# Kernel tuning notes

Hardware: AMD Instinct MI355X
Metric: run time of the kernel (lower is better)

## Reference

```python
import jax, jax.numpy as jnp
import numpy as np

SQRT_2_OVER_PI = 0.79788456

def gelu_tanh(x):
    # tanh-approximate GELU, matches torch F.gelu(approximate='tanh')
    return 0.5 * x * (1.0 + jnp.tanh(SQRT_2_OVER_PI * x * (1.0 + 0.044715 * x * x)))

def gelu_bwd(x):
    # analytical derivative of tanh-approx GELU (same constants as source)
    t = jnp.tanh(SQRT_2_OVER_PI * x * (1.0 + 0.044715 * x * x))
    return 0.5 * x * ((1.0 - t * t) * (SQRT_2_OVER_PI + 0.1070322243 * x * x)) + 0.5 * (1.0 + t)

def setup_inputs() -> dict:
    key = jax.random.key(0)
    ks = jax.random.split(key, 6)
    T, d_phi, d_h = 8192, 4096, 64
    d_mid = 4 * d_h
    return {
        "phi_seq": jax.random.normal(ks[0], (T, d_phi), jnp.float32),
        "C_seq": jax.random.uniform(ks[1], (T,), jnp.float32),
        "theta_K_w": jax.random.normal(ks[2], (d_h, d_phi), jnp.float32) * 0.02,
        "theta_Q_w": jax.random.normal(ks[3], (d_h, d_phi), jnp.float32) * 0.02,
        "W10": jax.random.normal(ks[4], (d_h, d_mid), jnp.float32) * 0.02,
        "b10": jnp.zeros((d_mid,), jnp.float32),
        "W20": jax.random.normal(ks[5], (d_mid,), jnp.float32) * 0.02,
        "b20": jnp.zeros((), jnp.float32),
        "log_eta": jnp.asarray(np.log(0.01), jnp.float32),
    }

def reference(phi_seq, C_seq, theta_K_w, theta_Q_w, W10, b10, W20, b20, log_eta):
    eta = jnp.exp(log_eta)
    # Slow-weight projections hoisted out of the scan (same math, one big GEMM)
    u_Q = phi_seq @ theta_Q_w.T  # [T, d_h]
    u_K = phi_seq @ theta_K_w.T  # [T, d_h]

    def step(carry, inp):
        W1, b1, W2, b2 = carry
        u_q, u_k = inp
        # score with current fast weights
        s = jax.nn.sigmoid(gelu_tanh(u_q @ W1 + b1) @ W2 + b2)
        # update fast weights (inner objective, C_t = 0.0)
        Z1 = u_k @ W1 + b1          # [d_mid]
        X2 = gelu_tanh(Z1)
        pred = jax.nn.sigmoid(X2 @ W2 + b2)
        d_Z2 = 2.0 * pred * pred * (1.0 - pred)  # d/dZ2 of (pred-0)^2
        d_Z1 = (d_Z2 * W2) * gelu_bwd(Z1)
        new_carry = (
            W1 - eta * jnp.outer(u_k, d_Z1),
            b1 - eta * d_Z1,
            W2 - eta * d_Z2 * X2,
            b2 - eta * d_Z2,
        )
        return new_carry, s

    _, scores = jax.lax.scan(step, (W10, b10, W20, b20), (u_Q, u_K))
    outer_loss = jnp.sum((scores - C_seq) ** 2)
    return scores, outer_loss
```

## Files before the change

### kernel.cpp

```cpp
#include <hip/hip_runtime.h>
#include <hip/hip_bf16.h>

#define DH 64
#define DM 256

typedef float f32x2 __attribute__((ext_vector_type(2)));

__device__ __forceinline__ f32x2 sp2(float s) { return (f32x2){s, s}; }
__device__ __forceinline__ f32x2 pkfma(f32x2 a, f32x2 b, f32x2 c) {
#if __has_builtin(__builtin_elementwise_fma)
    return __builtin_elementwise_fma(a, b, c);
#else
    f32x2 r; r.x = fmaf(a.x, b.x, c.x); r.y = fmaf(a.y, b.y, c.y); return r;
#endif
}

__device__ __forceinline__ float tanh_fast(float y) {
    float e = __expf(2.0f * y);
    return 1.0f - 2.0f / (e + 1.0f);
}
__device__ __forceinline__ float sigmoid_fast(float x) {
    return 1.0f / (1.0f + __expf(-x));
}

template <int CTRL, int RMASK>
__device__ __forceinline__ float dpp_term(float x) {
    int p = __builtin_amdgcn_update_dpp(0, __float_as_int(x), CTRL, RMASK, 0xf, false);
    return __int_as_float(p);
}
__device__ __forceinline__ float wave_sum63(float x) {
    x += dpp_term<0xB1,  0xf>(x);
    x += dpp_term<0x4E,  0xf>(x);
    x += dpp_term<0x141, 0xf>(x);
    x += dpp_term<0x140, 0xf>(x);
    x += dpp_term<0x142, 0xa>(x);
    x += dpp_term<0x143, 0xc>(x);
    return x;
}

__global__ __launch_bounds__(256) void proj_kernel(
    const float* __restrict__ phi,
    const float* __restrict__ thK,
    const float* __restrict__ thQ,
    float* __restrict__ u,
    int dphi)
{
    const int tid  = threadIdx.x;
    const int th32 = tid & 31;
    const int tt8  = tid >> 5;
    const int t0   = tt8 * 4;
    const int h0   = th32 * 4;
    const int T0   = blockIdx.x * 32;

    __shared__ float sPhiT[32][36];
    __shared__ float sThT[32][128];

    const int h   = tid >> 1;
    const int ko  = (tid & 1) * 16;
    const float* trow = (h < 64) ? (thQ + (size_t)h * dphi)
                                 : (thK + (size_t)(h - 64) * dphi);
    const int tr  = tid >> 3;
    const int k4p = (tid & 7) * 4;

    float4 pv, tv0, tv1, tv2, tv3;
    pv  = *(const float4*)&phi[(size_t)(T0 + tr) * dphi + k4p];
    tv0 = *(const float4*)&trow[ko + 0];
    tv1 = *(const float4*)&trow[ko + 4];
    tv2 = *(const float4*)&trow[ko + 8];
    tv3 = *(const float4*)&trow[ko + 12];

    float acc[4][4];
    #pragma unroll
    for (int i = 0; i < 4; ++i)
        #pragma unroll
        for (int jj = 0; jj < 4; ++jj) acc[i][jj] = 0.0f;

    const int NC = dphi / 32;
    for (int c = 0; c < NC; ++c) {
        __syncthreads();
        sPhiT[k4p + 0][tr] = pv.x;
        sPhiT[k4p + 1][tr] = pv.y;
        sPhiT[k4p + 2][tr] = pv.z;
        sPhiT[k4p + 3][tr] = pv.w;
        sThT[ko +  0][h] = tv0.x;  sThT[ko +  1][h] = tv0.y;
        sThT[ko +  2][h] = tv0.z;  sThT[ko +  3][h] = tv0.w;
        sThT[ko +  4][h] = tv1.x;  sThT[ko +  5][h] = tv1.y;
        sThT[ko +  6][h] = tv1.z;  sThT[ko +  7][h] = tv1.w;
        sThT[ko +  8][h] = tv2.x;  sThT[ko +  9][h] = tv2.y;
        sThT[ko + 10][h] = tv2.z;  sThT[ko + 11][h] = tv2.w;
        sThT[ko + 12][h] = tv3.x;  sThT[ko + 13][h] = tv3.y;
        sThT[ko + 14][h] = tv3.z;  sThT[ko + 15][h] = tv3.w;
        __syncthreads();
        if (c + 1 < NC) {
            const int kb = (c + 1) * 32;
            pv  = *(const float4*)&phi[(size_t)(T0 + tr) * dphi + kb + k4p];
            tv0 = *(const float4*)&trow[kb + ko + 0];
            tv1 = *(const float4*)&trow[kb + ko + 4];
            tv2 = *(const float4*)&trow[kb + ko + 8];
            tv3 = *(const float4*)&trow[kb + ko + 12];
        }
        #pragma unroll 8
        for (int k = 0; k < 32; ++k) {
            float4 ph = *(const float4*)&sPhiT[k][t0];
            float4 th = *(const float4*)&sThT[k][h0];
            acc[0][0] = fmaf(ph.x, th.x, acc[0][0]);
            acc[0][1] = fmaf(ph.x, th.y, acc[0][1]);
            acc[0][2] = fmaf(ph.x, th.z, acc[0][2]);
            acc[0][3] = fmaf(ph.x, th.w, acc[0][3]);
            acc[1][0] = fmaf(ph.y, th.x, acc[1][0]);
            acc[1][1] = fmaf(ph.y, th.y, acc[1][1]);
            acc[1][2] = fmaf(ph.y, th.z, acc[1][2]);
            acc[1][3] = fmaf(ph.y, th.w, acc[1][3]);
            acc[2][0] = fmaf(ph.z, th.x, acc[2][0]);
            acc[2][1] = fmaf(ph.z, th.y, acc[2][1]);
            acc[2][2] = fmaf(ph.z, th.z, acc[2][2]);
            acc[2][3] = fmaf(ph.z, th.w, acc[2][3]);
            acc[3][0] = fmaf(ph.w, th.x, acc[3][0]);
            acc[3][1] = fmaf(ph.w, th.y, acc[3][1]);
            acc[3][2] = fmaf(ph.w, th.z, acc[3][2]);
            acc[3][3] = fmaf(ph.w, th.w, acc[3][3]);
        }
    }
    #pragma unroll
    for (int i = 0; i < 4; ++i) {
        float4 o;
        o.x = acc[i][0]; o.y = acc[i][1]; o.z = acc[i][2]; o.w = acc[i][3];
        *(float4*)&u[(size_t)(T0 + t0 + i) * 128 + h0] = o;
    }
}

__global__ __launch_bounds__(256) void dots_kernel(
    const float* __restrict__ u, float4* __restrict__ dd4, int T)
{
    const int t    = (blockIdx.x * 256 + threadIdx.x) >> 6;
    const int lane = threadIdx.x & 63;
    if (t >= T) return;
    float uq = u[(size_t)t * 128 + lane];
    float uk = u[(size_t)t * 128 + 64 + lane];
    float k1 = (t >= 1) ? u[(size_t)(t - 1) * 128 + 64 + lane] : 0.f;
    float k2 = (t >= 2) ? u[(size_t)(t - 2) * 128 + 64 + lane] : 0.f;
    float a = k1 * uq, b = k1 * uk, c = k2 * uq, d = k2 * uk;
    #pragma unroll
    for (int off = 32; off > 0; off >>= 1) {
        a += __shfl_xor(a, off);
        b += __shfl_xor(b, off);
        c += __shfl_xor(c, off);
        d += __shfl_xor(d, off);
    }
    if (lane == 0) dd4[t] = make_float4(a, b, c, d);
}


#define ROWU(uqs, uks, ums, i2) do {                                         \
    f32x2 wa_ = pkfma(sp2(-(ums)), e1g0_, w1p[i2]);                          \
    f32x2 wb_ = pkfma(sp2(-(ums)), e1g1_, w1p[(i2) + 1]);                    \
    w1p[i2] = wa_; w1p[(i2) + 1] = wb_;                                      \
    aq0_ = pkfma(sp2(uqs), wa_, aq0_);  aq1_ = pkfma(sp2(uqs), wb_, aq1_);   \
    ak0_ = pkfma(sp2(uks), wa_, ak0_);  ak1_ = pkfma(sp2(uks), wb_, ak1_);   \
} while (0)
#define ROWU4(q4, k4, m4, b) do {                                            \
    ROWU((q4).x, (k4).x, (m4).x, (b) + 0);                                   \
    ROWU((q4).y, (k4).y, (m4).y, (b) + 2);                                   \
    ROWU((q4).z, (k4).z, (m4).z, (b) + 4);                                   \
    ROWU((q4).w, (k4).w, (m4).w, (b) + 6);                                   \
} while (0)
#define ROWM(uqs, uks, i2) do {                                              \
    aq0_ = pkfma(sp2(uqs), w1p[i2], aq0_);                                   \
    aq1_ = pkfma(sp2(uqs), w1p[(i2) + 1], aq1_);                             \
    ak0_ = pkfma(sp2(uks), w1p[i2], ak0_);                                   \
    ak1_ = pkfma(sp2(uks), w1p[(i2) + 1], ak1_);                             \
} while (0)
#define ROWM4(q4, k4, b) do {                                                \
    ROWM((q4).x, (k4).x, (b) + 0);                                           \
    ROWM((q4).y, (k4).y, (b) + 2);                                           \
    ROWM((q4).z, (k4).z, (b) + 4);                                           \
    ROWM((q4).w, (k4).w, (b) + 6);                                           \
} while (0)

#define STEP(t_) do {                                                        \
    const int pbR_ = (t_) & 1;                                               \
    const int r_   = (t_) & 63;                                              \
    const int B_   = (t_) >> 6;                                              \
    const int bs_  = B_ & 1;                                                 \
                                               \
    float4 pqQ_ = *(const float4*)&pqk[pbR_ ^ 1][0];                         \
    float4 pqK_ = *(const float4*)&pqk[pbR_ ^ 1][4];                         \
    const int sE_ = ((t_) + 2) & 3;                                          \
    float eb0_ = ebufT[sE_][0][lane];                                        \
    float eb1_ = ebufT[sE_][1][lane];                                        \
    float eb2_ = ebufT[sE_][2][lane];                                        \
    float eb3_ = ebufT[sE_][3][lane];                                        \
    float4 ddv_ = *(const float4*)&dbuf[bs_][r_][0];                         \
    float pA0_ = pbuf[pbR_][0][0][j], pA1_ = pbuf[pbR_][1][0][j];            \
    float pA2_ = pbuf[pbR_][2][0][j], pA3_ = pbuf[pbR_][3][0][j];            \
    float pB0_ = pbuf[pbR_][0][1][j], pB1_ = pbuf[pbR_][1][1][j];            \
    float pB2_ = pbuf[pbR_][2][1][j], pB3_ = pbuf[pbR_][3][1][j];            \
    const int ci_ = ((t_) > 0) ? (t_) - 1 : 0;                               \
    float cv_ = cbuf[((ci_ >> 6) & 1) * 64 + (ci_ & 63)];                    \
    const int rn_ = ((t_) + 1 < T) ? (t_) + 1 : T - 1;                       \
    const float* urN_ = &ubuf[((rn_ >> 6) & 1) * 8192 + (rn_ & 63) * 128];   \
    float4 q40_ = *(const float4*)&urN_[uqo +  0];                           \
    float4 q41_ = *(const float4*)&urN_[uqo +  4];                           \
    float4 q42_ = *(const float4*)&urN_[uqo +  8];                           \
    float4 q43_ = *(const float4*)&urN_[uqo + 12];                           \
    float4 k40_ = *(const float4*)&urN_[uko +  0];                           \
    float4 k41_ = *(const float4*)&urN_[uko +  4];                           \
    float4 k42_ = *(const float4*)&urN_[uko +  8];                           \
    float4 k43_ = *(const float4*)&urN_[uko + 12];                           \
    const int tm2_ = ((t_) >= 2) ? (t_) - 2 : 0;                             \
    const float* urM_ = &ubuf[((tm2_ >> 6) & 1) * 8192 + (tm2_ & 63) * 128]; \
    float4 m40_ = *(const float4*)&urM_[uko +  0];                           \
    float4 m41_ = *(const float4*)&urM_[uko +  4];                           \
    float4 m42_ = *(const float4*)&urM_[uko +  8];                           \
    float4 m43_ = *(const float4*)&urM_[uko + 12];                           \
                                            \
    float zs_ = ((pqQ_.x + pqQ_.y) + (pqQ_.z + pqQ_.w)) + b2;                \
    float zp_ = ((pqK_.x + pqK_.y) + (pqK_.z + pqK_.w)) + b2;                \
    float s_    = sigmoid_fast(zs_);                                         \
    float pred_ = sigmoid_fast(zp_);                                         \
    float dZ2_  = 2.f * pred_ * pred_ * (1.f - pred_);                       \
                  \
    f32x2 e1g0_ = sp2(dZ2p) * (f32x2){eb0_, eb1_};                           \
    f32x2 e1g1_ = sp2(dZ2p) * (f32x2){eb2_, eb3_};                           \
    f32x2 aq0_ = sp2(0.f), aq1_ = sp2(0.f), ak0_ = sp2(0.f), ak1_ = sp2(0.f);\
    ROWU4(q40_, k40_, m40_, 0);                                              \
    ROWU4(q41_, k41_, m41_, 8);                                              \
    ROWU4(q42_, k42_, m42_, 16);                                             \
    ROWU4(q43_, k43_, m43_, 24);                                             \
    { float4 wq_; wq_.x = aq0_.x; wq_.y = aq0_.y; wq_.z = aq1_.x; wq_.w = aq1_.y; \
      *(float4*)&pbuf[pbR_ ^ 1][wv][0][lane * 4] = wq_;                      \
      float4 wk_; wk_.x = ak0_.x; wk_.y = ak0_.y; wk_.z = ak1_.x; wk_.w = ak1_.y; \
      *(float4*)&pbuf[pbR_ ^ 1][wv][1][lane * 4] = wk_; }                    \
                                                    \
    float e1o_  = dZ2_ * en1;                                                \
    float e1o2_ = dZ2p * en2;                                                \
    b1j -= e1o_;                                                             \
    w2j  = fmaf(-eta * dZ2_, x2p, w2j);                                      \
    b2  -= eta * dZ2_;                                                       \
    float Pq_ = ((pA0_ + pA1_) + (pA2_ + pA3_));                             \
    float Pk_ = ((pB0_ + pB1_) + (pB2_ + pB3_));                             \
    float zq_ = Pq_ + b1j - e1o2_ * ddv_.z - e1o_ * ddv_.x;                  \
    float zk_ = Pk_ + b1j - e1o2_ * ddv_.w - e1o_ * ddv_.y;                  \
    float tk_ = tanh_fast(0.79788456f * zk_ * fmaf(0.044715f, zk_*zk_, 1.f));\
    float x2_ = 0.5f * zk_ * (1.f + tk_);                                    \
    float tq_ = tanh_fast(0.79788456f * zq_ * fmaf(0.044715f, zq_*zq_, 1.f));\
    float aq_ = 0.5f * zq_ * (1.f + tq_);                                    \
    float gb_ = 0.5f * zk_ * ((1.f - tk_*tk_) *                              \
                fmaf(0.1070322243f, zk_*zk_, 0.79788456f))                   \
              + 0.5f * (1.f + tk_);                                          \
    float en_ = eta * w2j * gb_;                                             \
    ebufT[(t_) & 3][j & 3][j >> 2] = en_;                                    \
    float pqs_ = wave_sum63(aq_ * w2j);                                      \
    float pks_ = wave_sum63(x2_ * w2j);                                      \
    if (lane == 63) { pqk[(t_) & 1][wv] = pqs_; pqk[(t_) & 1][4 + wv] = pks_; } \
    if ((t_) > 0) {                                                          \
        if (j == 0) out[(t_) - 1] = s_;                                      \
        float df_ = s_ - cv_;                                                \
        loss = fmaf(df_, df_, loss);                                         \
    }                                                                        \
    dZ2p = dZ2_; en2 = en1; en1 = en_; x2p = x2_;                            \
    if (r_ == 0 && B_ + 1 < NB) {                                            \
        const float* src_ = u + (size_t)(B_ + 1) * 8192;                     \
        _Pragma("unroll")                                                    \
        for (int q_ = 0; q_ < 8; ++q_)                                       \
            st[q_] = *(const float4*)&src_[q_ * 1024 + j * 4];               \
        if (j < 16) stc = *(const float4*)&C_seq[(B_ + 1) * 64 + j * 4];     \
        if (j < 64) std = dd_g4[(B_ + 1) * 64 + j];                          \
    }                                                                        \
    if (r_ == 32 && B_ + 1 < NB) {                                           \
        _Pragma("unroll")                                                    \
        for (int q_ = 0; q_ < 8; ++q_)                                       \
            *(float4*)&ubuf[(bs_ ^ 1) * 8192 + q_ * 1024 + j * 4] = st[q_];  \
        if (j < 16) *(float4*)&cbuf[(bs_ ^ 1) * 64 + j * 4] = stc;           \
        if (j < 64) *(float4*)&dbuf[bs_ ^ 1][j][0] = std;                    \
    }                                                                        \
    asm volatile("s_waitcnt lgkmcnt(0)" ::: "memory");                       \
    __builtin_amdgcn_s_barrier();                                            \
    asm volatile("" ::: "memory");                                           \
} while (0)

__global__ __launch_bounds__(256, 1) void ttt_scan(
    const float* __restrict__ u,
    const float4* __restrict__ dd_g4,
    const float* __restrict__ C_seq,
    const float* __restrict__ W10,
    const float* __restrict__ b10,
    const float* __restrict__ W20,
    const float* __restrict__ b20,
    const float* __restrict__ log_eta,
    float* __restrict__ out,
    int T)
{
    const int j    = threadIdx.x;
    const int lane = j & 63;
    const int wv   = j >> 6;
    const int uqo  = 16 * wv;
    const int uko  = 64 + 16 * wv;

    __shared__ __align__(16) float ubuf[2 * 8192];
    __shared__ __align__(16) float pbuf[2][4][2][256];
    __shared__ __align__(16) float ebufT[4][4][72];
    __shared__ __align__(16) float pqk[2][8];
    __shared__ __align__(16) float cbuf[2 * 64];
    __shared__ __align__(16) float dbuf[2][64][4];

    const int NB = T >> 6;

    #pragma unroll
    for (int q = 0; q < 8; ++q) {
        float4 v = *(const float4*)&u[q * 1024 + j * 4];
        *(float4*)&ubuf[q * 1024 + j * 4] = v;
    }
    if (j < 16) {
        float4 c4 = *(const float4*)&C_seq[j * 4];
        *(float4*)&cbuf[j * 4] = c4;
    }
    if (j < 64) *(float4*)&dbuf[0][j][0] = dd_g4[j];
    if (j < 8)  pqk[1][j] = -2.5e29f;
    {
        float* ez = &ebufT[2][0][0];
        for (int k = j; k < 2 * 4 * 72; k += 256) ez[k] = 0.f;
    }
    __syncthreads();

    f32x2 w1p[32];
    #pragma unroll
    for (int i = 0; i < 16; ++i) {
        float4 wr = *(const float4*)&W10[(16 * wv + i) * DM + lane * 4];
        w1p[2 * i]     = (f32x2){wr.x, wr.y};
        w1p[2 * i + 1] = (f32x2){wr.z, wr.w};
    }
    float b1j = b10[j];
    float w2j = W20[j];
    float b2  = b20[0];
    const float eta = __expf(log_eta[0]);
    float loss = 0.0f;
    float dZ2p = 0.0f, en1 = 0.0f, en2 = 0.0f, x2p = 0.0f;

    float4 st[8];
    float4 stc = make_float4(0.f, 0.f, 0.f, 0.f);
    float4 std = make_float4(0.f, 0.f, 0.f, 0.f);

    {
        const float* ur0 = &ubuf[0];
        float4 q40 = *(const float4*)&ur0[uqo +  0];
        float4 q41 = *(const float4*)&ur0[uqo +  4];
        float4 q42 = *(const float4*)&ur0[uqo +  8];
        float4 q43 = *(const float4*)&ur0[uqo + 12];
        float4 k40 = *(const float4*)&ur0[uko +  0];
        float4 k41 = *(const float4*)&ur0[uko +  4];
        float4 k42 = *(const float4*)&ur0[uko +  8];
        float4 k43 = *(const float4*)&ur0[uko + 12];
        f32x2 aq0_ = sp2(0.f), aq1_ = sp2(0.f), ak0_ = sp2(0.f), ak1_ = sp2(0.f);
        ROWM4(q40, k40, 0);
        ROWM4(q41, k41, 8);
        ROWM4(q42, k42, 16);
        ROWM4(q43, k43, 24);
        float4 wq; wq.x = aq0_.x; wq.y = aq0_.y; wq.z = aq1_.x; wq.w = aq1_.y;
        *(float4*)&pbuf[0][wv][0][lane * 4] = wq;
        float4 wk; wk.x = ak0_.x; wk.y = ak0_.y; wk.z = ak1_.x; wk.w = ak1_.y;
        *(float4*)&pbuf[0][wv][1][lane * 4] = wk;
    }
    __syncthreads();

    for (int t = 0; t < T; t += 2) {
        STEP(t);
        STEP(t + 1);
    }

    {
        float4 pqQ = *(const float4*)&pqk[(T - 1) & 1][0];
        float zs = ((pqQ.x + pqQ.y) + (pqQ.z + pqQ.w)) + b2;
        float s_ = sigmoid_fast(zs);
        const int ci = T - 1;
        float cv = cbuf[((ci >> 6) & 1) * 64 + (ci & 63)];
        float df = s_ - cv;
        loss = fmaf(df, df, loss);
        if (j == 0) { out[T - 1] = s_; out[T] = loss; }
    }
}

extern "C" void kernel_launch(void* const* d_in, const int* in_sizes, int n_in,
                              void* d_out, int out_size, void* d_ws, size_t ws_size,
                              hipStream_t stream) {
    const float* phi     = (const float*)d_in[0];
    const float* C_seq   = (const float*)d_in[1];
    const float* thK     = (const float*)d_in[2];
    const float* thQ     = (const float*)d_in[3];
    const float* W10     = (const float*)d_in[4];
    const float* b10     = (const float*)d_in[5];
    const float* W20     = (const float*)d_in[6];
    const float* b20     = (const float*)d_in[7];
    const float* log_eta = (const float*)d_in[8];

    const int T    = in_sizes[1];
    const int dphi = in_sizes[0] / T;

    float*  uw  = (float*)d_ws;
    float4* dd4 = (float4*)((char*)d_ws + (size_t)T * 128 * sizeof(float));

    proj_kernel<<<T / 32, 256, 0, stream>>>(phi, thK, thQ, uw, dphi);
    dots_kernel<<<T / 4, 256, 0, stream>>>(uw, dd4, T);
    ttt_scan<<<1, 256, 0, stream>>>(uw, dd4, C_seq, W10, b10, W20, b20, log_eta,
                                    (float*)d_out, T);
}
```

Before: 6.439 ms.

## Stream u rows from global memory into double-buffered registers instead of LDS

Removes the block-wise staging of the projected u rows, C_seq and dd vectors in shared memory, along with the periodic bulk copies and their LDS reads. Each step now issues global loads for the data needed two steps ahead into alternating register sets, so the loads overlap with one step of compute. This cuts LDS traffic and the staging work on the serial step loop. The cost is that global load latency must be hidden within roughly one step, which could stall the latency-bound recurrence, and register pressure goes up.

```diff
diff --git a/kernel.cpp b/kernel.cpp
--- a/kernel.cpp
+++ b/kernel.cpp
@@ -177,11 +177,24 @@
     ROWM((q4).w, (k4).w, (b) + 6);                                           \
 } while (0)
 
-#define STEP(t_) do {                                                        \
+#define STEP(t_, QC, QN, KC, KN, MC, MN, DDC, DDN, CC, CN) do {              \
     const int pbR_ = (t_) & 1;                                               \
-    const int r_   = (t_) & 63;                                              \
-    const int B_   = (t_) >> 6;                                              \
-    const int bs_  = B_ & 1;                                                 \
+          \
+    {                                                                        \
+        const int tn_ = ((t_) + 2 < T) ? (t_) + 2 : T - 1;                   \
+        const float4* upn_ = (const float4*)(u + (size_t)tn_ * 128);         \
+        QN[0] = upn_[uq4 + 0]; QN[1] = upn_[uq4 + 1];                        \
+        QN[2] = upn_[uq4 + 2]; QN[3] = upn_[uq4 + 3];                        \
+        KN[0] = upn_[uk4 + 0]; KN[1] = upn_[uk4 + 1];                        \
+        KN[2] = upn_[uk4 + 2]; KN[3] = upn_[uk4 + 3];                        \
+        const int tm_ = ((t_) >= 1) ? (t_) - 1 : 0;                          \
+        const float4* upm_ = (const float4*)(u + (size_t)tm_ * 128);         \
+        MN[0] = upm_[uk4 + 0]; MN[1] = upm_[uk4 + 1];                        \
+        MN[2] = upm_[uk4 + 2]; MN[3] = upm_[uk4 + 3];                        \
+        const int td_ = ((t_) + 1 < T) ? (t_) + 1 : T - 1;                   \
+        DDN = dd_g4[td_];                                                    \
+        CN  = C_seq[t_];                                                     \
+    }                                                                        \
                                                \
     float4 pqQ_ = *(const float4*)&pqk[pbR_ ^ 1][0];                         \
     float4 pqK_ = *(const float4*)&pqk[pbR_ ^ 1][4];                         \
@@ -190,29 +203,10 @@
     float eb1_ = ebufT[sE_][1][lane];                                        \
     float eb2_ = ebufT[sE_][2][lane];                                        \
     float eb3_ = ebufT[sE_][3][lane];                                        \
-    float4 ddv_ = *(const float4*)&dbuf[bs_][r_][0];                         \
     float pA0_ = pbuf[pbR_][0][0][j], pA1_ = pbuf[pbR_][1][0][j];            \
     float pA2_ = pbuf[pbR_][2][0][j], pA3_ = pbuf[pbR_][3][0][j];            \
     float pB0_ = pbuf[pbR_][0][1][j], pB1_ = pbuf[pbR_][1][1][j];            \
     float pB2_ = pbuf[pbR_][2][1][j], pB3_ = pbuf[pbR_][3][1][j];            \
-    const int ci_ = ((t_) > 0) ? (t_) - 1 : 0;                               \
-    float cv_ = cbuf[((ci_ >> 6) & 1) * 64 + (ci_ & 63)];                    \
-    const int rn_ = ((t_) + 1 < T) ? (t_) + 1 : T - 1;                       \
-    const float* urN_ = &ubuf[((rn_ >> 6) & 1) * 8192 + (rn_ & 63) * 128];   \
-    float4 q40_ = *(const float4*)&urN_[uqo +  0];                           \
-    float4 q41_ = *(const float4*)&urN_[uqo +  4];                           \
-    float4 q42_ = *(const float4*)&urN_[uqo +  8];                           \
-    float4 q43_ = *(const float4*)&urN_[uqo + 12];                           \
-    float4 k40_ = *(const float4*)&urN_[uko +  0];                           \
-    float4 k41_ = *(const float4*)&urN_[uko +  4];                           \
-    float4 k42_ = *(const float4*)&urN_[uko +  8];                           \
-    float4 k43_ = *(const float4*)&urN_[uko + 12];                           \
-    const int tm2_ = ((t_) >= 2) ? (t_) - 2 : 0;                             \
-    const float* urM_ = &ubuf[((tm2_ >> 6) & 1) * 8192 + (tm2_ & 63) * 128]; \
-    float4 m40_ = *(const float4*)&urM_[uko +  0];                           \
-    float4 m41_ = *(const float4*)&urM_[uko +  4];                           \
-    float4 m42_ = *(const float4*)&urM_[uko +  8];                           \
-    float4 m43_ = *(const float4*)&urM_[uko + 12];                           \
                                             \
     float zs_ = ((pqQ_.x + pqQ_.y) + (pqQ_.z + pqQ_.w)) + b2;                \
     float zp_ = ((pqK_.x + pqK_.y) + (pqK_.z + pqK_.w)) + b2;                \
@@ -223,10 +217,10 @@
     f32x2 e1g0_ = sp2(dZ2p) * (f32x2){eb0_, eb1_};                           \
     f32x2 e1g1_ = sp2(dZ2p) * (f32x2){eb2_, eb3_};                           \
     f32x2 aq0_ = sp2(0.f), aq1_ = sp2(0.f), ak0_ = sp2(0.f), ak1_ = sp2(0.f);\
-    ROWU4(q40_, k40_, m40_, 0);                                              \
-    ROWU4(q41_, k41_, m41_, 8);                                              \
-    ROWU4(q42_, k42_, m42_, 16);                                             \
-    ROWU4(q43_, k43_, m43_, 24);                                             \
+    ROWU4(QC[0], KC[0], MC[0], 0);                                           \
+    ROWU4(QC[1], KC[1], MC[1], 8);                                           \
+    ROWU4(QC[2], KC[2], MC[2], 16);                                          \
+    ROWU4(QC[3], KC[3], MC[3], 24);                                          \
     { float4 wq_; wq_.x = aq0_.x; wq_.y = aq0_.y; wq_.z = aq1_.x; wq_.w = aq1_.y; \
       *(float4*)&pbuf[pbR_ ^ 1][wv][0][lane * 4] = wq_;                      \
       float4 wk_; wk_.x = ak0_.x; wk_.y = ak0_.y; wk_.z = ak1_.x; wk_.w = ak1_.y; \
@@ -239,8 +233,8 @@
     b2  -= eta * dZ2_;                                                       \
     float Pq_ = ((pA0_ + pA1_) + (pA2_ + pA3_));                             \
     float Pk_ = ((pB0_ + pB1_) + (pB2_ + pB3_));                             \
-    float zq_ = Pq_ + b1j - e1o2_ * ddv_.z - e1o_ * ddv_.x;                  \
-    float zk_ = Pk_ + b1j - e1o2_ * ddv_.w - e1o_ * ddv_.y;                  \
+    float zq_ = Pq_ + b1j - e1o2_ * DDC.z - e1o_ * DDC.x;                    \
+    float zk_ = Pk_ + b1j - e1o2_ * DDC.w - e1o_ * DDC.y;                    \
     float tk_ = tanh_fast(0.79788456f * zk_ * fmaf(0.044715f, zk_*zk_, 1.f));\
     float x2_ = 0.5f * zk_ * (1.f + tk_);                                    \
     float tq_ = tanh_fast(0.79788456f * zq_ * fmaf(0.044715f, zq_*zq_, 1.f));\
@@ -255,25 +249,10 @@
     if (lane == 63) { pqk[(t_) & 1][wv] = pqs_; pqk[(t_) & 1][4 + wv] = pks_; } \
     if ((t_) > 0) {                                                          \
         if (j == 0) out[(t_) - 1] = s_;                                      \
-        float df_ = s_ - cv_;                                                \
+        float df_ = s_ - CC;                                                 \
         loss = fmaf(df_, df_, loss);                                         \
     }                                                                        \
     dZ2p = dZ2_; en2 = en1; en1 = en_; x2p = x2_;                            \
-    if (r_ == 0 && B_ + 1 < NB) {                                            \
-        const float* src_ = u + (size_t)(B_ + 1) * 8192;                     \
-        _Pragma("unroll")                                                    \
-        for (int q_ = 0; q_ < 8; ++q_)                                       \
-            st[q_] = *(const float4*)&src_[q_ * 1024 + j * 4];               \
-        if (j < 16) stc = *(const float4*)&C_seq[(B_ + 1) * 64 + j * 4];     \
-        if (j < 64) std = dd_g4[(B_ + 1) * 64 + j];                          \
-    }                                                                        \
-    if (r_ == 32 && B_ + 1 < NB) {                                           \
-        _Pragma("unroll")                                                    \
-        for (int q_ = 0; q_ < 8; ++q_)                                       \
-            *(float4*)&ubuf[(bs_ ^ 1) * 8192 + q_ * 1024 + j * 4] = st[q_];  \
-        if (j < 16) *(float4*)&cbuf[(bs_ ^ 1) * 64 + j * 4] = stc;           \
-        if (j < 64) *(float4*)&dbuf[bs_ ^ 1][j][0] = std;                    \
-    }                                                                        \
     asm volatile("s_waitcnt lgkmcnt(0)" ::: "memory");                       \
     __builtin_amdgcn_s_barrier();                                            \
     asm volatile("" ::: "memory");                                           \
@@ -294,34 +273,18 @@
     const int j    = threadIdx.x;
     const int lane = j & 63;
     const int wv   = j >> 6;
-    const int uqo  = 16 * wv;
-    const int uko  = 64 + 16 * wv;
-
-    __shared__ __align__(16) float ubuf[2 * 8192];
+    const int uq4  = 4 * wv;
+    const int uk4  = 16 + 4 * wv;
+
     __shared__ __align__(16) float pbuf[2][4][2][256];
     __shared__ __align__(16) float ebufT[4][4][72];
     __shared__ __align__(16) float pqk[2][8];
-    __shared__ __align__(16) float cbuf[2 * 64];
-    __shared__ __align__(16) float dbuf[2][64][4];
-
-    const int NB = T >> 6;
-
-    #pragma unroll
-    for (int q = 0; q < 8; ++q) {
-        float4 v = *(const float4*)&u[q * 1024 + j * 4];
-        *(float4*)&ubuf[q * 1024 + j * 4] = v;
-    }
-    if (j < 16) {
-        float4 c4 = *(const float4*)&C_seq[j * 4];
-        *(float4*)&cbuf[j * 4] = c4;
-    }
-    if (j < 64) *(float4*)&dbuf[0][j][0] = dd_g4[j];
+
     if (j < 8)  pqk[1][j] = -2.5e29f;
     {
         float* ez = &ebufT[2][0][0];
         for (int k = j; k < 2 * 4 * 72; k += 256) ez[k] = 0.f;
     }
-    __syncthreads();
 
     f32x2 w1p[32];
     #pragma unroll
@@ -337,20 +300,16 @@
     float loss = 0.0f;
     float dZ2p = 0.0f, en1 = 0.0f, en2 = 0.0f, x2p = 0.0f;
 
-    float4 st[8];
-    float4 stc = make_float4(0.f, 0.f, 0.f, 0.f);
-    float4 std = make_float4(0.f, 0.f, 0.f, 0.f);
+    float4 qA[4], qB[4], kA[4], kB[4], mA[4], mB[4];
+    float4 ddA, ddB;
+    float  cA, cB;
 
     {
-        const float* ur0 = &ubuf[0];
-        float4 q40 = *(const float4*)&ur0[uqo +  0];
-        float4 q41 = *(const float4*)&ur0[uqo +  4];
-        float4 q42 = *(const float4*)&ur0[uqo +  8];
-        float4 q43 = *(const float4*)&ur0[uqo + 12];
-        float4 k40 = *(const float4*)&ur0[uko +  0];
-        float4 k41 = *(const float4*)&ur0[uko +  4];
-        float4 k42 = *(const float4*)&ur0[uko +  8];
-        float4 k43 = *(const float4*)&ur0[uko + 12];
+        const float4* up0 = (const float4*)u;
+        float4 q40 = up0[uq4 + 0], q41 = up0[uq4 + 1];
+        float4 q42 = up0[uq4 + 2], q43 = up0[uq4 + 3];
+        float4 k40 = up0[uk4 + 0], k41 = up0[uk4 + 1];
+        float4 k42 = up0[uk4 + 2], k43 = up0[uk4 + 3];
         f32x2 aq0_ = sp2(0.f), aq1_ = sp2(0.f), ak0_ = sp2(0.f), ak1_ = sp2(0.f);
         ROWM4(q40, k40, 0);
         ROWM4(q41, k41, 8);
@@ -360,20 +319,30 @@
         *(float4*)&pbuf[0][wv][0][lane * 4] = wq;
         float4 wk; wk.x = ak0_.x; wk.y = ak0_.y; wk.z = ak1_.x; wk.w = ak1_.y;
         *(float4*)&pbuf[0][wv][1][lane * 4] = wk;
+
+        const int t1 = (T > 1) ? 1 : 0;
+        const float4* up1 = (const float4*)(u + (size_t)t1 * 128);
+        #pragma unroll
+        for (int i = 0; i < 4; ++i) {
+            qA[i] = up1[uq4 + i];
+            kA[i] = up1[uk4 + i];
+            mA[i] = make_float4(0.f, 0.f, 0.f, 0.f);
+        }
+        ddA = dd_g4[0];
+        cA  = C_seq[0];
     }
     __syncthreads();
 
     for (int t = 0; t < T; t += 2) {
-        STEP(t);
-        STEP(t + 1);
+        STEP(t,     qA, qB, kA, kB, mA, mB, ddA, ddB, cA, cB);
+        STEP(t + 1, qB, qA, kB, kA, mB, mA, ddB, ddA, cB, cA);
     }
 
     {
         float4 pqQ = *(const float4*)&pqk[(T - 1) & 1][0];
         float zs = ((pqQ.x + pqQ.y) + (pqQ.z + pqQ.w)) + b2;
         float s_ = sigmoid_fast(zs);
-        const int ci = T - 1;
-        float cv = cbuf[((ci >> 6) & 1) * 64 + (ci & 63)];
+        float cv = C_seq[T - 1];
         float df = s_ - cv;
         loss = fmaf(df, df, loss);
         if (j == 0) { out[T - 1] = s_; out[T] = loss; }
```

Measured after the change: 7.282 ms. 1.13x slower.
